# Kernel tuning notes

Measured on AMD Instinct MI355X. Metric: run time of the kernel, lower is better.

Reference implementation:

```python
import jax, jax.numpy as jnp
import numpy as np
import math

D = 1024
H = 16

def _new_gelu(x):
    return 0.5 * x * (1.0 + jnp.tanh(math.sqrt(2.0 / math.pi) * (x + 0.044715 * x ** 3)))

def _layer_norm(x, w):
    mu = jnp.mean(x, axis=-1, keepdims=True)
    var = jnp.var(x, axis=-1, keepdims=True)
    return (x - mu) * jax.lax.rsqrt(var + 1e-5) * w

def setup_inputs() -> dict:
    key = jax.random.key(0)
    ks = jax.random.split(key, 8)
    B, T = 2, 2048
    s = lambda fan_in: 1.0 / math.sqrt(fan_in)
    return {
        "x": jax.random.normal(ks[0], (B, T, D), jnp.float32),
        "ln1_w": jnp.ones((D,), jnp.float32),
        "attn_w": jax.random.normal(ks[1], (D, 3 * D), jnp.float32) * s(D),
        "attn_b": jnp.zeros((3 * D,), jnp.float32),
        "proj_w": jax.random.normal(ks[2], (D, D), jnp.float32) * s(D),
        "proj_b": jnp.zeros((D,), jnp.float32),
        "ln2_w": jnp.ones((D,), jnp.float32),
        "li1_w": jax.random.normal(ks[3], (D, 4 * D), jnp.float32) * s(D),
        "li1_b": jnp.zeros((4 * D,), jnp.float32),
        "li2_w": jax.random.normal(ks[4], (4 * D, D), jnp.float32) * s(4 * D),
        "li2_b": jnp.zeros((D,), jnp.float32),
    }

def reference(x, ln1_w, attn_w, attn_b, proj_w, proj_b, ln2_w, li1_w, li1_b, li2_w, li2_b):
    B, T, C = x.shape
    Dh = C // H
    # --- causal self-attention on pre-LN input ---
    h = _layer_norm(x, ln1_w)
    qkv = h @ attn_w + attn_b                      # [B,T,3C]
    q, k, v = jnp.split(qkv, 3, axis=-1)
    q = q.reshape(B, T, H, Dh)
    k = k.reshape(B, T, H, Dh)
    v = v.reshape(B, T, H, Dh)
    # NOTE: faithful to source — scale is 1/sqrt(BATCH), not 1/sqrt(head_dim)
    scale = 1.0 / math.sqrt(B)
    scores = jnp.einsum('bthd,bshd->bhts', q, k) * scale   # [B,H,T,T]
    causal = jnp.tril(jnp.ones((T, T), bool))
    scores = jnp.where(causal, scores, -jnp.inf)
    attn = jax.nn.softmax(scores, axis=-1)
    o = jnp.einsum('bhts,bshd->bthd', attn, v).reshape(B, T, C)
    x = x + o @ proj_w + proj_b
    # --- MLP ---
    h = _layer_norm(x, ln2_w)
    x = x + _new_gelu(h @ li1_w + li1_b) @ li2_w + li2_b
    return x
```

## Files before the change

### kernel.cpp

```cpp
#include <hip/hip_runtime.h>

typedef _Float16 f16;
typedef _Float16 f16x8 __attribute__((ext_vector_type(8)));
typedef _Float16 f16x4 __attribute__((ext_vector_type(4)));
typedef float    f32x4 __attribute__((ext_vector_type(4)));
typedef float    f32x16 __attribute__((ext_vector_type(16)));
typedef unsigned u32;
typedef unsigned u32x4 __attribute__((ext_vector_type(4)));

#define GAS __attribute__((address_space(1)))
#define LAS __attribute__((address_space(3)))

static __device__ __forceinline__ void gload_lds16(const void* g, void* l) {
    __builtin_amdgcn_global_load_lds((const GAS void*)g, (LAS void*)l, 16, 0, 0);
}

__global__ void wconv_t(const float* __restrict__ w, f16* __restrict__ wt, int K, int N) {
    __shared__ f16 t[32][33];
    const int tx = threadIdx.x, ty = threadIdx.y;
    const int n0 = blockIdx.x * 32, k0 = blockIdx.y * 32;
#pragma unroll
    for (int i = 0; i < 4; i++)
        t[ty + i * 8][tx] = (f16)w[(size_t)(k0 + ty + i * 8) * N + n0 + tx];
    __syncthreads();
#pragma unroll
    for (int i = 0; i < 4; i++)
        wt[(size_t)(n0 + ty + i * 8) * K + k0 + tx] = t[tx][ty + i * 8];
}

__global__ __launch_bounds__(256) void ln_kernel(const float* __restrict__ x,
                                                 const float* __restrict__ w,
                                                 f16* __restrict__ h) {
    const int row = blockIdx.x, tid = threadIdx.x;
    const float4 v = reinterpret_cast<const float4*>(x)[(size_t)row * 256 + tid];
    float s = v.x + v.y + v.z + v.w;
    float q = v.x * v.x + v.y * v.y + v.z * v.z + v.w * v.w;
#pragma unroll
    for (int m = 1; m < 64; m <<= 1) { s += __shfl_xor(s, m); q += __shfl_xor(q, m); }
    __shared__ float ss[4], qq[4];
    if ((tid & 63) == 0) { ss[tid >> 6] = s; qq[tid >> 6] = q; }
    __syncthreads();
    s = ss[0] + ss[1] + ss[2] + ss[3];
    q = qq[0] + qq[1] + qq[2] + qq[3];
    const float mu = s * (1.0f / 1024.0f);
    const float var = q * (1.0f / 1024.0f) - mu * mu;
    const float rs = rsqrtf(var + 1e-5f);
    const float4 wv = reinterpret_cast<const float4*>(w)[tid];
    f16x4 o;
    o[0] = (f16)((v.x - mu) * rs * wv.x);
    o[1] = (f16)((v.y - mu) * rs * wv.y);
    o[2] = (f16)((v.z - mu) * rs * wv.z);
    o[3] = (f16)((v.w - mu) * rs * wv.w);
    reinterpret_cast<f16x4*>(h)[(size_t)row * 256 + tid] = o;
}

__global__ __launch_bounds__(256) void vtrans(const f16* __restrict__ V, f16* __restrict__ Vt) {
    __shared__ f16 tl[64][72];
    const int tid = threadIdx.x;
    const int t0 = blockIdx.x * 64, bh = blockIdx.y;
    const int b = bh >> 4, hh = bh & 15;
    const int rr = tid >> 3, cc = (tid & 7) * 8;
#pragma unroll
    for (int p = 0; p < 2; p++) {
        f16x8 v = *(const f16x8*)(V + (size_t)(b * 2048 + t0 + p * 32 + rr) * 1024 + hh * 64 + cc);
#pragma unroll
        for (int j = 0; j < 8; j++) tl[p * 32 + rr][cc + j] = v[j];
    }
    __syncthreads();
#pragma unroll
    for (int p = 0; p < 2; p++) {
        const int d = p * 32 + rr;
        f16x8 o;
#pragma unroll
        for (int j = 0; j < 8; j++) o[j] = tl[cc + j][d];
        *(f16x8*)(Vt + (size_t)(bh * 64 + d) * 2048 + t0 + cc) = o;
    }
}

template <int EPI>
static __device__ __forceinline__ void gemm_epi(
    int gr, int gc, float v, int N, int gx,
    const float* bias, const float* res, void* outp,
    f16* oq, f16* ok, f16* ov, int bz, int BM) {
    if (EPI == 0) {
        if (gc < 1024)      oq[(size_t)gr * 1024 + gc]        = (f16)(v * 0.70710678118654752f);
        else if (gc < 2048) ok[(size_t)gr * 1024 + gc - 1024] = (f16)v;
        else                ov[(size_t)gr * 1024 + gc - 2048] = (f16)v;
    } else if (EPI == 1) {
        ((float*)outp)[(size_t)gr * N + gc] = v + res[(size_t)gr * N + gc];
    } else if (EPI == 2) {
        const float z = 0.7978845608028654f * (v + 0.044715f * v * v * v);
        const float t = 1.0f - 2.0f / (__builtin_amdgcn_exp2f(2.8853900817779268f * z) + 1.0f);
        ((f16*)outp)[(size_t)gr * N + gc] = (f16)(0.5f * v * (1.0f + t));
    } else {
        float* P = (float*)outp + (size_t)bz * ((size_t)gx * BM) * N;
        P[(size_t)gr * N + gc] = v;
    }
}

template <int EPI>
__global__ __launch_bounds__(256, 2) void gemm256(
    const f16* __restrict__ A, int lda,
    const f16* __restrict__ Bt, int ldb,
    const float* __restrict__ bias,
    const float* __restrict__ res,
    void* __restrict__ outp,
    f16* __restrict__ oq, f16* __restrict__ ok, f16* __restrict__ ov,
    int N, int K) {
    __shared__ alignas(16) f16 As[3][256 * 32];
    __shared__ alignas(16) f16 Bs[3][128 * 32];
    const int tid = threadIdx.x;
    const int lane = tid & 63, wv = tid >> 6;
    const int wr = wv >> 1, wc = wv & 1;
    const int m0 = blockIdx.x * 256, n0 = blockIdx.y * 128;
    const int l15 = lane & 15, lg = lane >> 4;

    f32x4 acc[8][4] = {};

    const int sr = tid >> 2;
    const int ss = (tid & 3) ^ ((tid >> 3) & 3);
    const size_t koff = (size_t)blockIdx.z * K;
    const f16* gA = A  + (size_t)(m0 + sr) * lda + ss * 8 + koff;
    const f16* gB = Bt + (size_t)(n0 + sr) * ldb + ss * 8 + koff;
    char* lA = (char*)As + tid * 16;
    char* lB = (char*)Bs + tid * 16;

    auto stage = [&](int buf, int k0) {
#pragma unroll
        for (int c = 0; c < 4; c++)
            gload_lds16(gA + (size_t)(c * 64) * lda + k0, lA + buf * 16384 + c * 4096);
#pragma unroll
        for (int c = 0; c < 2; c++)
            gload_lds16(gB + (size_t)(c * 64) * ldb + k0, lB + buf * 8192 + c * 4096);
    };
    auto compute = [&](int buf) {
        f16x8 af[8], bf[4];
#pragma unroll
        for (int i = 0; i < 8; i++) {
            const int ra = wr * 128 + i * 16 + l15;
            af[i] = *(const f16x8*)&As[buf][ra * 32 + ((lg ^ ((ra >> 1) & 3)) * 8)];
        }
#pragma unroll
        for (int i = 0; i < 4; i++) {
            const int rb = wc * 64 + i * 16 + l15;
            bf[i] = *(const f16x8*)&Bs[buf][rb * 32 + ((lg ^ ((rb >> 1) & 3)) * 8)];
        }
#pragma unroll
        for (int mi = 0; mi < 8; mi++)
#pragma unroll
            for (int ni = 0; ni < 4; ni++)
                acc[mi][ni] = __builtin_amdgcn_mfma_f32_16x16x32_f16(af[mi], bf[ni], acc[mi][ni], 0, 0, 0);
    };

    const int nk = K >> 5;
    stage(0, 0);
    if (nk > 1) {
        stage(1, 32);
        asm volatile("s_waitcnt vmcnt(6)" ::: "memory");
    } else {
        asm volatile("s_waitcnt vmcnt(0)" ::: "memory");
    }
    __builtin_amdgcn_s_barrier();

    for (int t = 0; t < nk; ++t) {
        const bool pref = (t + 2 < nk);
        if (pref) stage((t + 2) % 3, (t + 2) * 32);
        compute(t % 3);
        if (t + 1 < nk) {
            if (pref) asm volatile("s_waitcnt vmcnt(6)" ::: "memory");
            else      asm volatile("s_waitcnt vmcnt(0)" ::: "memory");
            __builtin_amdgcn_s_barrier();
        }
    }

#pragma unroll
    for (int mi = 0; mi < 8; mi++)
#pragma unroll
        for (int ni = 0; ni < 4; ni++) {
            const int gc = n0 + wc * 64 + ni * 16 + l15;
            const float bb = (EPI == 3) ? 0.0f : bias[gc];
#pragma unroll
            for (int r = 0; r < 4; r++) {
                const int gr = m0 + wr * 128 + mi * 16 + lg * 4 + r;
                gemm_epi<EPI>(gr, gc, acc[mi][ni][r] + bb, N, gridDim.x,
                              bias, res, outp, oq, ok, ov, blockIdx.z, 256);
            }
        }
}

template <int EPI>
__global__ __launch_bounds__(512) void gemm128(
    const f16* __restrict__ A, int lda,
    const f16* __restrict__ Bt, int ldb,
    const float* __restrict__ bias,
    const float* __restrict__ res,
    void* __restrict__ outp,
    f16* __restrict__ oq, f16* __restrict__ ok, f16* __restrict__ ov,
    int N, int K) {
    __shared__ alignas(16) f16 As[3][128 * 32];
    __shared__ alignas(16) f16 Bs[3][128 * 32];
    const int tid = threadIdx.x;
    const int lane = tid & 63, wv = tid >> 6;
    const int wr = wv >> 2, wc = wv & 3;
    const int m0 = blockIdx.x * 128, n0 = blockIdx.y * 128;
    const int l15 = lane & 15, lg = lane >> 4;

    f32x4 acc[4][2] = {};

    const int ar = tid >> 2;
    const int ac = (tid & 3) * 8;
    const size_t koff = (size_t)blockIdx.z * K;
    const f16* gA = A + (size_t)(m0 + ar) * lda + ac + koff;
    const f16* gB = Bt + (size_t)(n0 + ar) * ldb + ac + koff;
    char* lA0 = (char*)As + wv * 1024;
    char* lB0 = (char*)Bs + wv * 1024;

    auto stage = [&](int buf, int k0) {
        gload_lds16(gA + k0, lA0 + buf * 8192);
        gload_lds16(gB + k0, lB0 + buf * 8192);
    };
    auto compute = [&](int buf) {
        f16x8 af[4], bf[2];
#pragma unroll
        for (int i = 0; i < 4; i++)
            af[i] = *(const f16x8*)&As[buf][(wr * 64 + i * 16 + l15) * 32 + lg * 8];
#pragma unroll
        for (int n = 0; n < 2; n++)
            bf[n] = *(const f16x8*)&Bs[buf][(wc * 32 + n * 16 + l15) * 32 + lg * 8];
#pragma unroll
        for (int mi = 0; mi < 4; mi++)
#pragma unroll
            for (int ni = 0; ni < 2; ni++)
                acc[mi][ni] = __builtin_amdgcn_mfma_f32_16x16x32_f16(af[mi], bf[ni], acc[mi][ni], 0, 0, 0);
    };

    const int nk = K >> 5;
    stage(0, 0);
    if (nk > 1) {
        stage(1, 32);
        asm volatile("s_waitcnt vmcnt(2)" ::: "memory");
    } else {
        asm volatile("s_waitcnt vmcnt(0)" ::: "memory");
    }
    __builtin_amdgcn_s_barrier();

    for (int t = 0; t < nk; ++t) {
        const bool pref = (t + 2 < nk);
        if (pref) stage((t + 2) % 3, (t + 2) * 32);
        compute(t % 3);
        if (t + 1 < nk) {
            if (pref) asm volatile("s_waitcnt vmcnt(2)" ::: "memory");
            else      asm volatile("s_waitcnt vmcnt(0)" ::: "memory");
            __builtin_amdgcn_s_barrier();
        }
    }

#pragma unroll
    for (int mi = 0; mi < 4; mi++)
#pragma unroll
        for (int ni = 0; ni < 2; ni++) {
            const int gc = n0 + wc * 32 + ni * 16 + l15;
            const float bb = (EPI == 3) ? 0.0f : bias[gc];
#pragma unroll
            for (int r = 0; r < 4; r++) {
                const int gr = m0 + wr * 64 + mi * 16 + lg * 4 + r;
                gemm_epi<EPI>(gr, gc, acc[mi][ni][r] + bb, N, gridDim.x,
                              bias, res, outp, oq, ok, ov, blockIdx.z, 128);
            }
        }
}

__global__ __launch_bounds__(256) void kred(const float* __restrict__ p0,
                                            const float* __restrict__ p1,
                                            const float* __restrict__ bias,
                                            const float* __restrict__ res,
                                            float* __restrict__ out) {
    const size_t i = (size_t)blockIdx.x * 256 + threadIdx.x;
    const float4 a = ((const float4*)p0)[i];
    const float4 b = ((const float4*)p1)[i];
    const float4 r = ((const float4*)res)[i];
    const float4 w = ((const float4*)bias)[i & 255];
    float4 o;
    o.x = a.x + b.x + r.x + w.x;
    o.y = a.y + b.y + r.y + w.y;
    o.z = a.z + b.z + r.z + w.z;
    o.w = a.w + b.w + r.w + w.w;
    ((float4*)out)[i] = o;
}

__global__ __launch_bounds__(512) void attn_kernel(
    const f16* __restrict__ Q, const f16* __restrict__ Kb,
    const f16* __restrict__ Vt, f16* __restrict__ O) {
    __shared__ alignas(16) char pool[32768];
    const int tid = threadIdx.x, lane = tid & 63, w = tid >> 6;
    const int l31 = lane & 31, hi = lane >> 5;
    const int bx = blockIdx.x;
    const int qs = bx >> 5, bh = bx & 31;
    const int b = bh >> 4, hh = bh & 15;
    const int qtile = w * 8 + qs;
    const int q0 = qtile * 32;
    const int last = qtile >> 1;
    const int nk = ((56 + qs) >> 1) + 1;

    const f16* qrow = Q + (size_t)(b * 2048 + q0 + l31) * 1024 + hh * 64 + hi * 8;
    f16x8 qf[4];
#pragma unroll
    for (int s = 0; s < 4; s++) qf[s] = *(const f16x8*)(qrow + s * 16);

    f32x16 oacc[2] = {};
    float m = -3e38f, l = 0.0f;

    const int srow = tid >> 3, sslot = (tid & 7) ^ ((tid >> 3) & 7);
    const f16* kg = Kb + ((size_t)b * 2048 + srow) * 1024 + hh * 64 + sslot * 8;
    const f16* vg = Vt + ((size_t)bh * 64 + srow) * 2048 + sslot * 8;
    char* kld = pool + tid * 16;
    char* vld = pool + 8192 + tid * 16;

    auto stage = [&](int buf, int kt) {
        gload_lds16(kg + (size_t)kt * 65536, kld + buf * 16384);
        gload_lds16(vg + kt * 64, vld + buf * 16384);
    };

    const int rs = l31 & 7;

    auto tilestep = [&](int buf, bool diag) {
        const f16* Kbuf = (const f16*)(pool + buf * 16384);
        const f16* Vbuf = (const f16*)(pool + buf * 16384 + 8192);
        const bool doH1 = !diag || (qtile & 1);
        const int triH = qtile & 1;

        f16x8 k0[4], k1[4];
#pragma unroll
        for (int s = 0; s < 4; s++)
            k0[s] = *(const f16x8*)&Kbuf[l31 * 64 + (((s * 2 + hi) ^ rs) * 8)];
        if (doH1)
#pragma unroll
            for (int s = 0; s < 4; s++)
                k1[s] = *(const f16x8*)&Kbuf[(32 + l31) * 64 + (((s * 2 + hi) ^ rs) * 8)];

        f32x16 sacc0 = {}, sacc1 = {};
        __builtin_amdgcn_s_setprio(1);
#pragma unroll
        for (int s = 0; s < 4; s++)
            sacc0 = __builtin_amdgcn_mfma_f32_32x32x16_f16(k0[s], qf[s], sacc0, 0, 0, 0);
        if (doH1)
#pragma unroll
            for (int s = 0; s < 4; s++)
                sacc1 = __builtin_amdgcn_mfma_f32_32x32x16_f16(k1[s], qf[s], sacc1, 0, 0, 0);
        __builtin_amdgcn_s_setprio(0);

        if (diag) {
            if (triH == 0) {
#pragma unroll
                for (int r = 0; r < 16; r++) {
                    const int keyoff = (r & 3) + 8 * (r >> 2) + 4 * hi;
                    sacc0[r] = (keyoff > l31) ? -3e38f : sacc0[r];
                }
            } else {
#pragma unroll
                for (int r = 0; r < 16; r++) {
                    const int keyoff = (r & 3) + 8 * (r >> 2) + 4 * hi;
                    sacc1[r] = (keyoff > l31) ? -3e38f : sacc1[r];
                }
            }
        }
        float t8[8];
#pragma unroll
        for (int i = 0; i < 8; i++) t8[i] = fmaxf(sacc0[2 * i], sacc0[2 * i + 1]);
        if (doH1)
#pragma unroll
            for (int i = 0; i < 8; i++) t8[i] = fmaxf(t8[i], fmaxf(sacc1[2 * i], sacc1[2 * i + 1]));
#pragma unroll
        for (int i = 0; i < 4; i++) t8[i] = fmaxf(t8[i], t8[i + 4]);
        float tm = fmaxf(fmaxf(t8[0], t8[1]), fmaxf(t8[2], t8[3]));
        tm = fmaxf(tm, __shfl_xor(tm, 32));
        const bool up = tm > m + 8.0f;
        if (__any(up)) {
            const float mnew = up ? tm : m;
            const float alpha = __expf(m - mnew);
            m = mnew;
            l *= alpha;
#pragma unroll
            for (int r = 0; r < 16; r++) { oacc[0][r] *= alpha; oacc[1][r] *= alpha; }
        }
        const float mref = m * 1.44269504f;

        float psum = 0.0f;
        u32 wd[8];
        {
            float p[16];
#pragma unroll
            for (int r = 0; r < 16; r++)
                p[r] = __builtin_amdgcn_exp2f(sacc0[r] * 1.44269504f - mref);
            float s8[8];
#pragma unroll
            for (int i = 0; i < 8; i++) s8[i] = p[2 * i] + p[2 * i + 1];
#pragma unroll
            for (int i = 0; i < 4; i++) s8[i] = s8[i] + s8[i + 4];
            psum += (s8[0] + s8[1]) + (s8[2] + s8[3]);
#pragma unroll
            for (int i = 0; i < 8; i++)
                wd[i] = __builtin_bit_cast(u32, __builtin_amdgcn_cvt_pkrtz(p[2 * i], p[2 * i + 1]));
        }
        const u32 e0 = __shfl_xor(hi ? wd[0] : wd[2], 32);
        const u32 e1 = __shfl_xor(hi ? wd[1] : wd[3], 32);
        const u32 e2 = __shfl_xor(hi ? wd[4] : wd[6], 32);
        const u32 e3 = __shfl_xor(hi ? wd[5] : wd[7], 32);
        u32x4 c0, c1;
        c0[0] = hi ? e0 : wd[0]; c0[1] = hi ? e1 : wd[1];
        c0[2] = hi ? wd[2] : e0; c0[3] = hi ? wd[3] : e1;
        c1[0] = hi ? e2 : wd[4]; c1[1] = hi ? e3 : wd[5];
        c1[2] = hi ? wd[6] : e2; c1[3] = hi ? wd[7] : e3;
        const f16x8 pb00 = __builtin_bit_cast(f16x8, c0);
        const f16x8 pb01 = __builtin_bit_cast(f16x8, c1);

        f16x8 vfa, vfb;
        __builtin_amdgcn_s_setprio(1);
        vfa = *(const f16x8*)&Vbuf[l31 * 64 + ((hi ^ rs) * 8)];
        vfb = *(const f16x8*)&Vbuf[l31 * 64 + (((2 + hi) ^ rs) * 8)];
        oacc[0] = __builtin_amdgcn_mfma_f32_32x32x16_f16(vfa, pb00, oacc[0], 0, 0, 0);
        oacc[0] = __builtin_amdgcn_mfma_f32_32x32x16_f16(vfb, pb01, oacc[0], 0, 0, 0);
        vfa = *(const f16x8*)&Vbuf[(32 + l31) * 64 + ((hi ^ rs) * 8)];
        vfb = *(const f16x8*)&Vbuf[(32 + l31) * 64 + (((2 + hi) ^ rs) * 8)];
        oacc[1] = __builtin_amdgcn_mfma_f32_32x32x16_f16(vfa, pb00, oacc[1], 0, 0, 0);
        oacc[1] = __builtin_amdgcn_mfma_f32_32x32x16_f16(vfb, pb01, oacc[1], 0, 0, 0);
        __builtin_amdgcn_s_setprio(0);

        if (doH1) {
            float p[16];
#pragma unroll
            for (int r = 0; r < 16; r++)
                p[r] = __builtin_amdgcn_exp2f(sacc1[r] * 1.44269504f - mref);
            float s8[8];
#pragma unroll
            for (int i = 0; i < 8; i++) s8[i] = p[2 * i] + p[2 * i + 1];
#pragma unroll
            for (int i = 0; i < 4; i++) s8[i] = s8[i] + s8[i + 4];
            psum += (s8[0] + s8[1]) + (s8[2] + s8[3]);
#pragma unroll
            for (int i = 0; i < 8; i++)
                wd[i] = __builtin_bit_cast(u32, __builtin_amdgcn_cvt_pkrtz(p[2 * i], p[2 * i + 1]));
            const u32 f0 = __shfl_xor(hi ? wd[0] : wd[2], 32);
            const u32 f1 = __shfl_xor(hi ? wd[1] : wd[3], 32);
            const u32 f2 = __shfl_xor(hi ? wd[4] : wd[6], 32);
            const u32 f3 = __shfl_xor(hi ? wd[5] : wd[7], 32);
            u32x4 d0, d1;
            d0[0] = hi ? f0 : wd[0]; d0[1] = hi ? f1 : wd[1];
            d0[2] = hi ? wd[2] : f0; d0[3] = hi ? wd[3] : f1;
            d1[0] = hi ? f2 : wd[4]; d1[1] = hi ? f3 : wd[5];
            d1[2] = hi ? wd[6] : f2; d1[3] = hi ? wd[7] : f3;
            const f16x8 pb10 = __builtin_bit_cast(f16x8, d0);
            const f16x8 pb11 = __builtin_bit_cast(f16x8, d1);

            __builtin_amdgcn_s_setprio(1);
            vfa = *(const f16x8*)&Vbuf[l31 * 64 + (((4 + hi) ^ rs) * 8)];
            vfb = *(const f16x8*)&Vbuf[l31 * 64 + (((6 + hi) ^ rs) * 8)];
            oacc[0] = __builtin_amdgcn_mfma_f32_32x32x16_f16(vfa, pb10, oacc[0], 0, 0, 0);
            oacc[0] = __builtin_amdgcn_mfma_f32_32x32x16_f16(vfb, pb11, oacc[0], 0, 0, 0);
            vfa = *(const f16x8*)&Vbuf[(32 + l31) * 64 + (((4 + hi) ^ rs) * 8)];
            vfb = *(const f16x8*)&Vbuf[(32 + l31) * 64 + (((6 + hi) ^ rs) * 8)];
            oacc[1] = __builtin_amdgcn_mfma_f32_32x32x16_f16(vfa, pb10, oacc[1], 0, 0, 0);
            oacc[1] = __builtin_amdgcn_mfma_f32_32x32x16_f16(vfb, pb11, oacc[1], 0, 0, 0);
            __builtin_amdgcn_s_setprio(0);
        }
        psum += __shfl_xor(psum, 32);
        l += psum;
    };

    stage(0, 0);
    asm volatile("s_waitcnt vmcnt(0)" ::: "memory");
    __builtin_amdgcn_s_barrier();
    int buf = 0;
    for (int t = 0; t < nk; ++t) {
        if (t + 1 < nk) stage(buf ^ 1, t + 1);
        if (t <= last) tilestep(buf, t == last);
        asm volatile("s_waitcnt vmcnt(0)" ::: "memory");
        __builtin_amdgcn_s_barrier();
        buf ^= 1;
    }

    const float inv = 1.0f / l;
    f16* ot = (f16*)pool + (w & 3) * (32 * 72);
#pragma unroll
    for (int g = 0; g < 2; g++) {
        if ((w >> 2) == g) {
#pragma unroll
            for (int dt = 0; dt < 2; dt++)
#pragma unroll
                for (int r = 0; r < 16; r++) {
                    const int d = dt * 32 + (r & 3) + 8 * (r >> 2) + 4 * hi;
                    ot[l31 * 72 + d] = (f16)(oacc[dt][r] * inv);
                }
            asm volatile("s_waitcnt lgkmcnt(0)" ::: "memory");
#pragma unroll
            for (int i = 0; i < 4; i++) {
                const int row = i * 8 + (lane >> 3), col = (lane & 7) * 8;
                const f16x8 o8 = *(const f16x8*)&ot[row * 72 + col];
                *(f16x8*)(O + (size_t)(b * 2048 + q0 + row) * 1024 + hh * 64 + col) = o8;
            }
        }
        __syncthreads();
    }
}

extern "C" void kernel_launch(void* const* d_in, const int* in_sizes, int n_in,
                              void* d_out, int out_size, void* d_ws, size_t ws_size,
                              hipStream_t stream) {
    const float* x      = (const float*)d_in[0];
    const float* ln1_w  = (const float*)d_in[1];
    const float* attn_w = (const float*)d_in[2];
    const float* attn_b = (const float*)d_in[3];
    const float* proj_w = (const float*)d_in[4];
    const float* proj_b = (const float*)d_in[5];
    const float* ln2_w  = (const float*)d_in[6];
    const float* li1_w  = (const float*)d_in[7];
    const float* li1_b  = (const float*)d_in[8];
    const float* li2_w  = (const float*)d_in[9];
    const float* li2_b  = (const float*)d_in[10];
    float* out = (float*)d_out;

    char* ws = (char*)d_ws;
    size_t off = 0;
    auto alloc = [&](size_t bytes) { void* p = ws + off; off += (bytes + 255) & ~(size_t)255; return p; };
    f16* W1t = (f16*)alloc((size_t)3072 * 1024 * 2);
    f16* W2t = (f16*)alloc((size_t)1024 * 1024 * 2);
    f16* W3t = (f16*)alloc((size_t)4096 * 1024 * 2);
    f16* W4t = (f16*)alloc((size_t)1024 * 4096 * 2);
    f16* h   = (f16*)alloc((size_t)4096 * 1024 * 2);
    f16* Qb  = (f16*)alloc((size_t)4096 * 1024 * 2);
    f16* Kb  = (f16*)alloc((size_t)4096 * 1024 * 2);
    f16* Vb  = (f16*)alloc((size_t)4096 * 1024 * 2);
    f16* Vt  = (f16*)alloc((size_t)4096 * 1024 * 2);
    f16* Ob  = (f16*)alloc((size_t)4096 * 1024 * 2);
    float* x1 = (float*)alloc((size_t)4096 * 1024 * 4);
    float* P  = (float*)alloc((size_t)2 * 4096 * 1024 * 4);
    f16* Ab = Qb;

    dim3 b328(32, 8);
    wconv_t<<<dim3(96, 32),  b328, 0, stream>>>(attn_w, W1t, 1024, 3072);
    wconv_t<<<dim3(32, 32),  b328, 0, stream>>>(proj_w, W2t, 1024, 1024);
    wconv_t<<<dim3(128, 32), b328, 0, stream>>>(li1_w,  W3t, 1024, 4096);
    wconv_t<<<dim3(32, 128), b328, 0, stream>>>(li2_w,  W4t, 4096, 1024);

    ln_kernel<<<4096, 256, 0, stream>>>(x, ln1_w, h);
    gemm256<0><<<dim3(16, 24), 256, 0, stream>>>(h, 1024, W1t, 1024, attn_b, nullptr,
                                                 nullptr, Qb, Kb, Vb, 3072, 1024);
    vtrans<<<dim3(32, 32), 256, 0, stream>>>(Vb, Vt);
    attn_kernel<<<256, 512, 0, stream>>>(Qb, Kb, Vt, Ob);
    gemm128<1><<<dim3(32, 8), 512, 0, stream>>>(Ob, 1024, W2t, 1024, proj_b, x,
                                                x1, nullptr, nullptr, nullptr, 1024, 1024);
    ln_kernel<<<4096, 256, 0, stream>>>(x1, ln2_w, h);
    gemm256<2><<<dim3(16, 32), 256, 0, stream>>>(h, 1024, W3t, 1024, li1_b, nullptr,
                                                 Ab, nullptr, nullptr, nullptr, 4096, 1024);
    gemm128<3><<<dim3(32, 8, 2), 512, 0, stream>>>(Ab, 4096, W4t, 4096, nullptr, nullptr,
                                                   P, nullptr, nullptr, nullptr, 1024, 2048);
    kred<<<4096, 256, 0, stream>>>(P, P + (size_t)4096 * 1024, li2_b, x1, out);
}
```

Before: 262.2 us.

## Restructure gemm256 into 256x256 tiles with 8 waves and quarter-staged pipeline

gemm256 now uses 512 threads and 256x256 output tiles with a K-step of 64. Each K tile is split into four quarter stages (two for B, two for A) in a double-buffered 128KB shared pool. Global-to-LDS loads are interleaved with MFMA compute at quarter granularity, and s_setprio raises wave priority during the MFMA bursts. The aim is more data reuse per block and a finer-grained overlap of loads with compute. In exchange the grids get smaller (fewer blocks for the QKV and MLP-up GEMMs), and the large LDS footprint likely limits each CU to one block despite the launch bound of 2.

```diff
diff --git a/kernel.cpp b/kernel.cpp
--- a/kernel.cpp
+++ b/kernel.cpp
@@ -10,6 +10,8 @@
 
 #define GAS __attribute__((address_space(1)))
 #define LAS __attribute__((address_space(3)))
+
+template <int N> struct IC { static constexpr int v = N; };
 
 static __device__ __forceinline__ void gload_lds16(const void* g, void* l) {
     __builtin_amdgcn_global_load_lds((const GAS void*)g, (LAS void*)l, 16, 0, 0);
@@ -99,7 +101,7 @@
 }
 
 template <int EPI>
-__global__ __launch_bounds__(256, 2) void gemm256(
+__global__ __launch_bounds__(512, 2) void gemm256(
     const f16* __restrict__ A, int lda,
     const f16* __restrict__ Bt, int ldb,
     const float* __restrict__ bias,
@@ -107,71 +109,106 @@
     void* __restrict__ outp,
     f16* __restrict__ oq, f16* __restrict__ ok, f16* __restrict__ ov,
     int N, int K) {
-    __shared__ alignas(16) f16 As[3][256 * 32];
-    __shared__ alignas(16) f16 Bs[3][128 * 32];
+    __shared__ alignas(16) f16 pool[8 * 8192];
     const int tid = threadIdx.x;
     const int lane = tid & 63, wv = tid >> 6;
-    const int wr = wv >> 1, wc = wv & 1;
-    const int m0 = blockIdx.x * 256, n0 = blockIdx.y * 128;
+    const int wr = wv >> 2, wc = wv & 3;
+    const int m0 = blockIdx.x * 256, n0 = blockIdx.y * 256;
     const int l15 = lane & 15, lg = lane >> 4;
+    const int sw = (l15 >> 1) & 3;
 
     f32x4 acc[8][4] = {};
-
-    const int sr = tid >> 2;
-    const int ss = (tid & 3) ^ ((tid >> 3) & 3);
-    const size_t koff = (size_t)blockIdx.z * K;
-    const f16* gA = A  + (size_t)(m0 + sr) * lda + ss * 8 + koff;
-    const f16* gB = Bt + (size_t)(n0 + sr) * ldb + ss * 8 + koff;
-    char* lA = (char*)As + tid * 16;
-    char* lB = (char*)Bs + tid * 16;
-
-    auto stage = [&](int buf, int k0) {
-#pragma unroll
-        for (int c = 0; c < 4; c++)
-            gload_lds16(gA + (size_t)(c * 64) * lda + k0, lA + buf * 16384 + c * 4096);
-#pragma unroll
-        for (int c = 0; c < 2; c++)
-            gload_lds16(gB + (size_t)(c * 64) * ldb + k0, lB + buf * 8192 + c * 4096);
-    };
-    auto compute = [&](int buf) {
-        f16x8 af[8], bf[4];
-#pragma unroll
-        for (int i = 0; i < 8; i++) {
-            const int ra = wr * 128 + i * 16 + l15;
-            af[i] = *(const f16x8*)&As[buf][ra * 32 + ((lg ^ ((ra >> 1) & 3)) * 8)];
-        }
-#pragma unroll
-        for (int i = 0; i < 4; i++) {
-            const int rb = wc * 64 + i * 16 + l15;
-            bf[i] = *(const f16x8*)&Bs[buf][rb * 32 + ((lg ^ ((rb >> 1) & 3)) * 8)];
-        }
-#pragma unroll
-        for (int mi = 0; mi < 8; mi++)
+    f16x8 bf[4][2];
+
+    const f16* aSrc[2][2];
+    const f16* bSrc[2][2];
+#pragma unroll
+    for (int c = 0; c < 2; c++) {
+        const int lr = (tid >> 3) + c * 64;
+        const int sl = (tid & 3) ^ ((lr >> 1) & 3);
+        const int colb = ((tid >> 2) & 1) * 32 + sl * 8;
+#pragma unroll
+        for (int h = 0; h < 2; h++) {
+            const int ar = ((lr >> 5) << 6) + h * 32 + (lr & 31);
+            aSrc[c][h] = A + (size_t)(m0 + ar) * lda + colb;
+            const int br = ((lr >> 6) << 7) + h * 64 + (lr & 63);
+            bSrc[c][h] = Bt + (size_t)(n0 + br) * ldb + colb;
+        }
+    }
+    f16* ldst = pool + tid * 8;
+
+    auto stageQ = [&](int par, int qid, int kt) {
+        f16* d = ldst + (par * 4 + qid) * 8192;
+        if (qid >= 2) {
+            gload_lds16(aSrc[0][qid - 2] + kt * 64, d);
+            gload_lds16(aSrc[1][qid - 2] + kt * 64, d + 4096);
+        } else {
+            gload_lds16(bSrc[0][qid] + kt * 64, d);
+            gload_lds16(bSrc[1][qid] + kt * 64, d + 4096);
+        }
+    };
+
+    const f16* aBase = pool + (size_t)(wr * 2) * 2048 + l15 * 64 + (lg ^ sw) * 8;
+    const f16* bBase = pool + (wc & 1) * 8192 + (size_t)((wc >> 1) * 64 + l15) * 64 + (lg ^ sw) * 8;
+
+    auto loadB = [&](int par) {
+        const f16* bb = bBase + par * 32768;
+#pragma unroll
+        for (int ni = 0; ni < 4; ni++)
+#pragma unroll
+            for (int kk = 0; kk < 2; kk++)
+                bf[ni][kk] = *(const f16x8*)(bb + ni * 1024 + kk * 32);
+    };
+    auto computeQ = [&](int par, auto qc) {
+        constexpr int Q = decltype(qc)::v;
+        const f16* ab = aBase + par * 32768 + (2 + (Q & 1)) * 8192 + (Q >> 1) * 2048;
+        f16x8 af[2][2];
+#pragma unroll
+        for (int mi2 = 0; mi2 < 2; mi2++)
+#pragma unroll
+            for (int kk = 0; kk < 2; kk++)
+                af[mi2][kk] = *(const f16x8*)(ab + mi2 * 1024 + kk * 32);
+        __builtin_amdgcn_s_setprio(1);
+#pragma unroll
+        for (int mi2 = 0; mi2 < 2; mi2++)
 #pragma unroll
             for (int ni = 0; ni < 4; ni++)
-                acc[mi][ni] = __builtin_amdgcn_mfma_f32_16x16x32_f16(af[mi], bf[ni], acc[mi][ni], 0, 0, 0);
-    };
-
-    const int nk = K >> 5;
-    stage(0, 0);
-    if (nk > 1) {
-        stage(1, 32);
-        asm volatile("s_waitcnt vmcnt(6)" ::: "memory");
-    } else {
-        asm volatile("s_waitcnt vmcnt(0)" ::: "memory");
-    }
-    __builtin_amdgcn_s_barrier();
-
-    for (int t = 0; t < nk; ++t) {
-        const bool pref = (t + 2 < nk);
-        if (pref) stage((t + 2) % 3, (t + 2) * 32);
-        compute(t % 3);
-        if (t + 1 < nk) {
-            if (pref) asm volatile("s_waitcnt vmcnt(6)" ::: "memory");
-            else      asm volatile("s_waitcnt vmcnt(0)" ::: "memory");
-            __builtin_amdgcn_s_barrier();
-        }
-    }
+#pragma unroll
+                for (int kk = 0; kk < 2; kk++)
+                    acc[Q * 2 + mi2][ni] = __builtin_amdgcn_mfma_f32_16x16x32_f16(
+                        af[mi2][kk], bf[ni][kk], acc[Q * 2 + mi2][ni], 0, 0, 0);
+        __builtin_amdgcn_s_setprio(0);
+    };
+
+#define VMW(n) asm volatile("s_waitcnt vmcnt(" #n ")" ::: "memory"); __builtin_amdgcn_s_barrier()
+
+    const int nt = K >> 6;
+    stageQ(0, 0, 0); stageQ(0, 1, 0); stageQ(0, 2, 0); stageQ(0, 3, 0);
+    stageQ(1, 0, 1);
+    VMW(6);
+
+    for (int kt = 0; kt < nt - 2; ++kt) {
+        const int par = kt & 1, parn = par ^ 1;
+        stageQ(parn, 1, kt + 1); VMW(6); loadB(par); computeQ(par, IC<0>{});
+        stageQ(parn, 2, kt + 1); VMW(6); computeQ(par, IC<1>{});
+        stageQ(parn, 3, kt + 1); VMW(6); computeQ(par, IC<2>{});
+        stageQ(par, 0, kt + 2);  VMW(6); computeQ(par, IC<3>{});
+    }
+    {
+        const int kt = nt - 2, par = kt & 1, parn = par ^ 1;
+        stageQ(parn, 1, kt + 1); VMW(6); loadB(par); computeQ(par, IC<0>{});
+        stageQ(parn, 2, kt + 1); VMW(6); computeQ(par, IC<1>{});
+        stageQ(parn, 3, kt + 1); VMW(6); computeQ(par, IC<2>{});
+        VMW(4); computeQ(par, IC<3>{});
+    }
+    {
+        const int par = (nt - 1) & 1;
+        VMW(2); loadB(par); computeQ(par, IC<0>{});
+        VMW(0); computeQ(par, IC<1>{});
+        computeQ(par, IC<2>{});
+        computeQ(par, IC<3>{});
+    }
+#undef VMW
 
 #pragma unroll
     for (int mi = 0; mi < 8; mi++)
@@ -543,14 +580,14 @@
     wconv_t<<<dim3(32, 128), b328, 0, stream>>>(li2_w,  W4t, 4096, 1024);
 
     ln_kernel<<<4096, 256, 0, stream>>>(x, ln1_w, h);
-    gemm256<0><<<dim3(16, 24), 256, 0, stream>>>(h, 1024, W1t, 1024, attn_b, nullptr,
+    gemm256<0><<<dim3(16, 12), 512, 0, stream>>>(h, 1024, W1t, 1024, attn_b, nullptr,
                                                  nullptr, Qb, Kb, Vb, 3072, 1024);
     vtrans<<<dim3(32, 32), 256, 0, stream>>>(Vb, Vt);
     attn_kernel<<<256, 512, 0, stream>>>(Qb, Kb, Vt, Ob);
     gemm128<1><<<dim3(32, 8), 512, 0, stream>>>(Ob, 1024, W2t, 1024, proj_b, x,
                                                 x1, nullptr, nullptr, nullptr, 1024, 1024);
     ln_kernel<<<4096, 256, 0, stream>>>(x1, ln2_w, h);
-    gemm256<2><<<dim3(16, 32), 256, 0, stream>>>(h, 1024, W3t, 1024, li1_b, nullptr,
+    gemm256<2><<<dim3(16, 16), 512, 0, stream>>>(h, 1024, W3t, 1024, li1_b, nullptr,
                                                  Ab, nullptr, nullptr, nullptr, 4096, 1024);
     gemm128<3><<<dim3(32, 8, 2), 512, 0, stream>>>(Ab, 4096, W4t, 4096, nullptr, nullptr,
                                                    P, nullptr, nullptr, nullptr, 1024, 2048);
```

After: 249.7 us. 4.8% less time.
